# Optimization experiments

Hardware: AMD Instinct MI355X
Metric: run time of the kernel (lower is better)

## Reference

```python
import jax, jax.numpy as jnp
import numpy as np

NUM_EVENT, EVENT_DIM = 6, 32
NUM_WORD, WORD_DIM = 100000, 128
NUM_SKU, SKU_DIM = 500000, 128
NUM_CAT, CAT_DIM = 10000, 64
NUM_PRICE, PRICE_DIM = 100, 32
NUM_URL, URL_DIM = 200000, 128
HIDDEN = 512
B, S, W = 256, 256, 12
PAD = 0


def _table(key, n, d):
    t = jax.random.normal(key, (n, d), dtype=jnp.float32) * 0.02
    return t.at[PAD].set(0.0)  # padding_idx row is zero


def setup_inputs() -> dict:
    key = jax.random.key(0)
    ks = jax.random.split(key, 20)
    inp = {
        "event_table": _table(ks[0], NUM_EVENT, EVENT_DIM),
        "word_table": _table(ks[1], NUM_WORD, WORD_DIM),
        "sku_table": _table(ks[2], NUM_SKU, SKU_DIM),
        "cat_table": _table(ks[3], NUM_CAT, CAT_DIM),
        "price_table": _table(ks[4], NUM_PRICE, PRICE_DIM),
        "url_table": _table(ks[5], NUM_URL, URL_DIM),
        # Linear weights, torch convention: y = x @ W.T + b
        "sku_w": jax.random.normal(ks[6], (HIDDEN, EVENT_DIM + SKU_DIM + CAT_DIM + PRICE_DIM + WORD_DIM), dtype=jnp.float32) * 0.02,
        "sku_b": jnp.zeros((HIDDEN,), dtype=jnp.float32),
        "url_w": jax.random.normal(ks[7], (HIDDEN, URL_DIM + EVENT_DIM), dtype=jnp.float32) * 0.02,
        "url_b": jnp.zeros((HIDDEN,), dtype=jnp.float32),
        "query_w": jax.random.normal(ks[8], (HIDDEN, EVENT_DIM + WORD_DIM), dtype=jnp.float32) * 0.02,
        "query_b": jnp.zeros((HIDDEN,), dtype=jnp.float32),
        "event_type": jax.random.randint(ks[9], (B, S), 0, NUM_EVENT, dtype=jnp.int32),
        "sku_id": jax.random.randint(ks[10], (B, S), 0, NUM_SKU, dtype=jnp.int32),
        "url_id": jax.random.randint(ks[11], (B, S), 0, NUM_URL, dtype=jnp.int32),
        "cat_id": jax.random.randint(ks[12], (B, S), 0, NUM_CAT, dtype=jnp.int32),
        "price_id": jax.random.randint(ks[13], (B, S), 0, NUM_PRICE, dtype=jnp.int32),
        "word_id": jax.random.randint(ks[14], (B, S, W), 0, NUM_WORD, dtype=jnp.int32),
    }
    return inp


def _linear_relu(x, w, b):
    return jax.nn.relu(jnp.einsum("bsi,hi->bsh", x, w) + b)


def reference(event_table, word_table, sku_table, cat_table, price_table, url_table,
              sku_w, sku_b, url_w, url_b, query_w, query_b,
              event_type, sku_id, url_id, cat_id, price_id, word_id):
    # padding mask: 1.0 where event_type == PAD_IDX
    src_padding_mask = (event_type == PAD).astype(jnp.float32)

    event_emb = event_table[event_type]                 # [B,S,E]
    word_emb = word_table[word_id].mean(axis=-2)        # [B,S,Wd] (WordEmbedding avg)

    # SKU branch (event types 1,2,3): concat(event, sku, cat, price, word)
    sku_in = jnp.concatenate([event_emb, sku_table[sku_id], cat_table[cat_id],
                              price_table[price_id], word_emb], axis=-1)
    sku_out = _linear_relu(sku_in, sku_w, sku_b)        # [B,S,H]

    # URL branch (event type 4): concat(url, event)  -- note order in UrlEmbedding
    url_in = jnp.concatenate([url_table[url_id], event_emb], axis=-1)
    url_out = _linear_relu(url_in, url_w, url_b)

    # Query branch (event type 5): concat(event, word)
    query_in = jnp.concatenate([event_emb, word_emb], axis=-1)
    query_out = _linear_relu(query_in, query_w, query_b)

    is_sku = ((event_type >= 1) & (event_type <= 3))[..., None]
    is_url = (event_type == 4)[..., None]
    is_query = (event_type == 5)[..., None]

    seq_emb = (jnp.where(is_sku, sku_out, 0.0)
               + jnp.where(is_url, url_out, 0.0)
               + jnp.where(is_query, query_out, 0.0))   # PAD positions stay zero
    return seq_emb, src_padding_mask
```

## Files before the change

kernel.cpp:

```cpp
#include <hip/hip_runtime.h>
#include <hip/hip_bf16.h>
#if !__has_builtin(__builtin_amdgcn_cvt_pk_fp8_f32) || !__has_builtin(__builtin_amdgcn_cvt_pk_f32_fp8)
#include <hip/hip_fp8.h>
#endif

#define CUR_OFF   0
#define SLOT_OFF  1024
#define POS_OFF   263168
#define WSKU_OFF  1049600
#define WURL_OFF  1442816
#define WQRY_OFF  1639424
#define WF8_OFF   2097152
#define XS_OFF    27697152
#define XU_OFF    78127104
#define XQ_OFF    103342080

#define NPOS      65536
#define OUT_MASK  33554432
#define F8_SCALE  64.0f
#define F8_INV    (1.0f / (12.0f * 64.0f))

typedef __attribute__((ext_vector_type(8))) short bf16x8;
typedef __attribute__((ext_vector_type(4))) float f32x4;
typedef __attribute__((ext_vector_type(2))) float f32x2;
typedef __attribute__((ext_vector_type(2))) unsigned int u32x2;

__device__ __forceinline__ unsigned short f2bf(float x) {
    unsigned int u = __float_as_uint(x);
    return (unsigned short)((u + 0x7fffu + ((u >> 16) & 1u)) >> 16);
}
__device__ __forceinline__ void st2(__hip_bfloat16* d, float2 v) {
    unsigned int pk = (unsigned int)f2bf(v.x) | ((unsigned int)f2bf(v.y) << 16);
    *reinterpret_cast<unsigned int*>(d) = pk;
}
__device__ __forceinline__ float2 ld2(const float* p) {
    return *reinterpret_cast<const float2*>(p);
}

__device__ __forceinline__ unsigned int pk4_fp8(float a, float b, float c, float d) {
#if __has_builtin(__builtin_amdgcn_cvt_pk_fp8_f32)
    unsigned int v = 0;
    v = __builtin_amdgcn_cvt_pk_fp8_f32(a, b, v, false);
    v = __builtin_amdgcn_cvt_pk_fp8_f32(c, d, v, true);
    return v;
#else
    __hip_fp8_e4m3 fa(a), fb(b), fc(c), fd(d);
    return (unsigned int)fa.__x | ((unsigned int)fb.__x << 8)
         | ((unsigned int)fc.__x << 16) | ((unsigned int)fd.__x << 24);
#endif
}
__device__ __forceinline__ float2 upk2_fp8(unsigned int u) {
#if __has_builtin(__builtin_amdgcn_cvt_pk_f32_fp8)
    f32x2 r = __builtin_amdgcn_cvt_pk_f32_fp8(u, false);
    return make_float2(r.x, r.y);
#else
    __hip_fp8_e4m3 fa, fb;
    fa.__x = (unsigned char)(u & 0xff);
    fb.__x = (unsigned char)((u >> 8) & 0xff);
    return make_float2((float)fa, (float)fb);
#endif
}

#define AS1(p) ((const __attribute__((address_space(1))) void*)(p))
#define AS3(p) ((__attribute__((address_space(3))) void*)(p))

__global__ __launch_bounds__(256) void prep_k(const float* __restrict__ sw,
                                              const float* __restrict__ uw,
                                              const float* __restrict__ qw,
                                              const float* __restrict__ word_t,
                                              char* ws) {
    const int b = blockIdx.x, t = threadIdx.x;
    if (b < 6250) {
        size_t i = ((size_t)b * 256 + t) * 8;
        f32x4 v0 = *reinterpret_cast<const f32x4*>(word_t + i);
        f32x4 v1 = *reinterpret_cast<const f32x4*>(word_t + i + 4);
        u32x2 pk;
        pk.x = pk4_fp8(v0.x * F8_SCALE, v0.y * F8_SCALE, v0.z * F8_SCALE, v0.w * F8_SCALE);
        pk.y = pk4_fp8(v1.x * F8_SCALE, v1.y * F8_SCALE, v1.z * F8_SCALE, v1.w * F8_SCALE);
        *reinterpret_cast<u32x2*>((unsigned char*)(ws + WF8_OFF) + i) = pk;
        return;
    }
    int tt = (b - 6250) * 256 + t;
    if (tt < 3) ((int*)(ws + CUR_OFF))[tt] = 0;
    if (tt < 196608) {
        ((unsigned short*)(ws + WSKU_OFF))[tt] = f2bf(sw[tt]);
    } else if (tt < 294912) {
        int i = tt - 196608; int n = i / 192, k = i % 192;
        ((unsigned short*)(ws + WURL_OFF))[i] = (k < 160) ? f2bf(uw[n * 160 + k]) : 0;
    } else {
        int i = tt - 294912; int n = i / 192, k = i % 192;
        ((unsigned short*)(ws + WQRY_OFF))[i] = (k < 160) ? f2bf(qw[n * 160 + k]) : 0;
    }
}

__global__ __launch_bounds__(256) void alloc_k(const int* __restrict__ et_a,
                                               float* __restrict__ out, char* ws) {
    __shared__ int s_wcnt[4][3];
    __shared__ int s_base[3];
    __shared__ int s_woff[4][3];
    const int t = threadIdx.x, lane = t & 63, wid = t >> 6;
    int p = blockIdx.x * 256 + t;
    int et = et_a[p];
    int br = (et >= 1 && et <= 3) ? 0 : (et == 4 ? 1 : (et == 5 ? 2 : -1));
    unsigned long long m0 = __ballot(br == 0);
    unsigned long long m1 = __ballot(br == 1);
    unsigned long long m2 = __ballot(br == 2);
    if (lane == 0) {
        s_wcnt[wid][0] = (int)__popcll(m0);
        s_wcnt[wid][1] = (int)__popcll(m1);
        s_wcnt[wid][2] = (int)__popcll(m2);
    }
    __syncthreads();
    if (t < 3) {
        int c0 = s_wcnt[0][t], c1 = s_wcnt[1][t], c2 = s_wcnt[2][t], c3 = s_wcnt[3][t];
        int tot = c0 + c1 + c2 + c3;
        s_base[t] = tot ? atomicAdd(&((int*)(ws + CUR_OFF))[t], tot) : 0;
        s_woff[0][t] = 0; s_woff[1][t] = c0; s_woff[2][t] = c0 + c1; s_woff[3][t] = c0 + c1 + c2;
    }
    __syncthreads();
    unsigned long long lt = (1ull << lane) - 1ull;
    int slot = -1;
    if (br == 0)      slot = s_base[0] + s_woff[wid][0] + (int)__popcll(m0 & lt);
    else if (br == 1) slot = s_base[1] + s_woff[wid][1] + (int)__popcll(m1 & lt);
    else if (br == 2) slot = s_base[2] + s_woff[wid][2] + (int)__popcll(m2 & lt);
    ((int*)(ws + SLOT_OFF))[p] = slot;
    if (slot >= 0) ((int*)(ws + POS_OFF))[br * NPOS + slot] = p;
    __builtin_nontemporal_store((et == 0) ? 1.0f : 0.0f, &out[OUT_MASK + p]);
}

__device__ __forceinline__ float2 wmean_f8(const unsigned char* __restrict__ wt8,
                                           const int* __restrict__ wids, int lane) {
    float sx = 0.f, sy = 0.f;
    #pragma unroll
    for (int k = 0; k < 12; ++k) {
        unsigned int u = *reinterpret_cast<const unsigned short*>(
            wt8 + (size_t)wids[k] * 128 + 2 * lane);
        float2 v = upk2_fp8(u);
        sx += v.x; sy += v.y;
    }
    return make_float2(sx * F8_INV, sy * F8_INV);
}

__global__ __launch_bounds__(256) void build_k(
    const float* __restrict__ ev_t,
    const float* __restrict__ sku_t,  const float* __restrict__ cat_t,
    const float* __restrict__ price_t,const float* __restrict__ url_t,
    const int* __restrict__ et_a,     const int* __restrict__ sku_id,
    const int* __restrict__ url_id,   const int* __restrict__ cat_id,
    const int* __restrict__ price_id, const int* __restrict__ word_id,
    float* __restrict__ out, char* ws)
{
    const int t = threadIdx.x, lane = t & 63, wid = t >> 6;
    const int p = blockIdx.x * 4 + wid;
    const int et = et_a[p];
    if (et == 0) {
        f32x4 z = {0.f, 0.f, 0.f, 0.f};
        float* orow = out + (size_t)p * 512;
        __builtin_nontemporal_store(z, reinterpret_cast<f32x4*>(&orow[lane * 8]));
        __builtin_nontemporal_store(z, reinterpret_cast<f32x4*>(&orow[lane * 8 + 4]));
        return;
    }
    const int slot = ((const int*)(ws + SLOT_OFF))[p];
    const unsigned char* wf8 = (const unsigned char*)(ws + WF8_OFF);
    const float* evr = ev_t + et * 32;
    if (et <= 3) {
        __hip_bfloat16* X = (__hip_bfloat16*)(ws + XS_OFF + (size_t)slot * 768);
        if (lane < 16) st2(X + 2 * lane, ld2(evr + 2 * lane));
        const float* sr = sku_t + (size_t)sku_id[p] * 128;
        st2(X + 32 + 2 * lane, ld2(sr + 2 * lane));
        const float* crr = cat_t + (size_t)cat_id[p] * 64;
        if (lane < 32) st2(X + 160 + 2 * lane, ld2(crr + 2 * lane));
        const float* prr = price_t + (size_t)price_id[p] * 32;
        if (lane < 16) st2(X + 224 + 2 * lane, ld2(prr + 2 * lane));
        float2 w = wmean_f8(wf8, word_id + (size_t)p * 12, lane);
        st2(X + 256 + 2 * lane, w);
    } else if (et == 4) {
        __hip_bfloat16* X = (__hip_bfloat16*)(ws + XU_OFF + (size_t)slot * 384);
        const float* ur = url_t + (size_t)url_id[p] * 128;
        st2(X + 2 * lane, ld2(ur + 2 * lane));
        if (lane < 16) st2(X + 128 + 2 * lane, ld2(evr + 2 * lane));
        if (lane < 16) st2(X + 160 + 2 * lane, make_float2(0.f, 0.f));
    } else {
        __hip_bfloat16* X = (__hip_bfloat16*)(ws + XQ_OFF + (size_t)slot * 384);
        if (lane < 16) st2(X + 2 * lane, ld2(evr + 2 * lane));
        float2 w = wmean_f8(wf8, word_id + (size_t)p * 12, lane);
        st2(X + 32 + 2 * lane, w);
        if (lane < 16) st2(X + 160 + 2 * lane, make_float2(0.f, 0.f));
    }
}

__global__ __launch_bounds__(256, 2) void gemm_all_k(
    const char* __restrict__ ws_c, const float* __restrict__ sku_b,
    const float* __restrict__ url_b, const float* __restrict__ qry_b,
    float* __restrict__ out)
{
    const int z = blockIdx.z;
    const int count = ((const int*)(ws_c + CUR_OFF))[z];
    const int nmt = (count + 127) >> 7;
    const int nwg = nmt * 4;
    const int orig = blockIdx.x;
    if (orig >= nwg) return;
    const int q8 = nwg >> 3, r8 = nwg & 7;
    const int xcd = orig & 7, idx = orig >> 3;
    const int wg = (xcd < r8 ? xcd * (q8 + 1) : r8 * (q8 + 1) + (xcd - r8) * q8) + idx;
    const int mt = wg >> 2;
    const int row0 = mt * 128;
    const int nc0  = (wg & 3) * 128;

    const char* arena; const char* Wb; const float* bias; const int* posm;
    int astride, nkt;
    if (z == 0) { arena = ws_c + XS_OFF; Wb = ws_c + WSKU_OFF; bias = sku_b;
                  posm = (const int*)(ws_c + POS_OFF);          astride = 768; nkt = 6; }
    else if (z == 1) { arena = ws_c + XU_OFF; Wb = ws_c + WURL_OFF; bias = url_b;
                  posm = (const int*)(ws_c + POS_OFF) + NPOS;   astride = 384; nkt = 3; }
    else       { arena = ws_c + XQ_OFF; Wb = ws_c + WQRY_OFF; bias = qry_b;
                  posm = (const int*)(ws_c + POS_OFF) + 2*NPOS; astride = 384; nkt = 3; }
    const int wstride = astride;

    __shared__ char lds[2][2][16384];

    const int t = threadIdx.x;
    const int lane = t & 63;
    const int wid  = t >> 6;
    const int wr = wid >> 1, wc = wid & 1;
    const int r = lane & 15, q = lane >> 4;

    auto stage = [&](int buf, int kt) {
        #pragma unroll
        for (int i = 0; i < 4; ++i) {
            int row = i * 32 + (t >> 3);
            int sb  = (t & 7) ^ (row & 7);
            const char* ga = arena + (size_t)(row0 + row) * astride + kt * 128 + sb * 16;
            __builtin_amdgcn_global_load_lds(AS1(ga), AS3(&lds[buf][0][i * 4096 + t * 16]), 16, 0, 0);
            const char* gb = Wb + (size_t)(nc0 + row) * wstride + kt * 128 + sb * 16;
            __builtin_amdgcn_global_load_lds(AS1(gb), AS3(&lds[buf][1][i * 4096 + t * 16]), 16, 0, 0);
        }
    };

    f32x4 acc[4][4];
    #pragma unroll
    for (int m = 0; m < 4; ++m)
        #pragma unroll
        for (int n = 0; n < 4; ++n)
            acc[m][n] = (f32x4){0.f, 0.f, 0.f, 0.f};

    stage(0, 0);
    __syncthreads();
    int cur = 0;
    for (int kt = 0; kt < nkt; ++kt) {
        if (kt + 1 < nkt) stage(cur ^ 1, kt + 1);
        #pragma unroll
        for (int kk = 0; kk < 2; ++kk) {
            bf16x8 af[4], bfr[4];
            #pragma unroll
            for (int m = 0; m < 4; ++m) {
                int arow = wr * 64 + m * 16 + r;
                af[m] = *reinterpret_cast<const bf16x8*>(
                    &lds[cur][0][arow * 128 + (((kk * 4 + q) ^ (r & 7)) * 16)]);
            }
            #pragma unroll
            for (int n = 0; n < 4; ++n) {
                int brow = wc * 64 + n * 16 + r;
                bfr[n] = *reinterpret_cast<const bf16x8*>(
                    &lds[cur][1][brow * 128 + (((kk * 4 + q) ^ (r & 7)) * 16)]);
            }
            #pragma unroll
            for (int m = 0; m < 4; ++m)
                #pragma unroll
                for (int n = 0; n < 4; ++n)
                    acc[m][n] = __builtin_amdgcn_mfma_f32_16x16x32_bf16(af[m], bfr[n], acc[m][n], 0, 0, 0);
        }
        __syncthreads();
        cur ^= 1;
    }

    float bv[4];
    #pragma unroll
    for (int n = 0; n < 4; ++n) bv[n] = bias[nc0 + wc * 64 + n * 16 + r];
    #pragma unroll
    for (int m = 0; m < 4; ++m) {
        #pragma unroll
        for (int j = 0; j < 4; ++j) {
            int rl = wr * 64 + m * 16 + q * 4 + j;
            int gr = row0 + rl;
            if (gr < count) {
                int pos = posm[gr];
                float* orow = out + (size_t)pos * 512 + nc0 + wc * 64;
                #pragma unroll
                for (int n = 0; n < 4; ++n)
                    __builtin_nontemporal_store(fmaxf(acc[m][n][j] + bv[n], 0.f),
                                                &orow[n * 16 + r]);
            }
        }
    }
}

extern "C" void kernel_launch(void* const* d_in, const int* in_sizes, int n_in,
                              void* d_out, int out_size, void* d_ws, size_t ws_size,
                              hipStream_t stream) {
    const float* ev_t    = (const float*)d_in[0];
    const float* word_t  = (const float*)d_in[1];
    const float* sku_t   = (const float*)d_in[2];
    const float* cat_t   = (const float*)d_in[3];
    const float* price_t = (const float*)d_in[4];
    const float* url_t   = (const float*)d_in[5];
    const float* sku_w   = (const float*)d_in[6];
    const float* sku_b   = (const float*)d_in[7];
    const float* url_w   = (const float*)d_in[8];
    const float* url_b   = (const float*)d_in[9];
    const float* query_w = (const float*)d_in[10];
    const float* query_b = (const float*)d_in[11];
    const int* event_type = (const int*)d_in[12];
    const int* sku_id     = (const int*)d_in[13];
    const int* url_id     = (const int*)d_in[14];
    const int* cat_id     = (const int*)d_in[15];
    const int* price_id   = (const int*)d_in[16];
    const int* word_id    = (const int*)d_in[17];

    char*  ws  = (char*)d_ws;
    float* out = (float*)d_out;

    prep_k<<<7786, 256, 0, stream>>>(sku_w, url_w, query_w, word_t, ws);
    alloc_k<<<256, 256, 0, stream>>>(event_type, out, ws);
    build_k<<<16384, 256, 0, stream>>>(ev_t, sku_t, cat_t, price_t, url_t,
                                       event_type, sku_id, url_id, cat_id, price_id,
                                       word_id, out, ws);
    dim3 gg(2048, 1, 3);
    gemm_all_k<<<gg, 256, 0, stream>>>(ws, sku_b, url_b, query_b, out);
}
```

Measured before the change: 92.79 us.

## Switch GEMM operands and weights from bf16 to scaled fp8 MFMA

Activations (gathered embeddings) and all three weight matrices are now quantized to fp8 e4m3 with a x64 scale instead of bf16, and the GEMM uses the fp8 16x16x32 MFMA with a 1/4096 rescale in the epilogue. This halves workspace traffic for the X arenas and weights, halves K-tiles per GEMM, and raises MFMA throughput. The cost is much lower precision on every GEMM operand, including the embeddings themselves, which may exceed tolerance.

```diff
diff --git a/kernel.cpp b/kernel.cpp
--- a/kernel.cpp
+++ b/kernel.cpp
@@ -8,19 +8,18 @@
 #define SLOT_OFF  1024
 #define POS_OFF   263168
 #define WSKU_OFF  1049600
-#define WURL_OFF  1442816
-#define WQRY_OFF  1639424
+#define WURL_OFF  1246208
+#define WQRY_OFF  1377280
 #define WF8_OFF   2097152
-#define XS_OFF    27697152
-#define XU_OFF    78127104
-#define XQ_OFF    103342080
+#define XS_OFF    16777216
+#define XU_OFF    50331648
+#define XQ_OFF    68157440
 
 #define NPOS      65536
 #define OUT_MASK  33554432
 #define F8_SCALE  64.0f
-#define F8_INV    (1.0f / (12.0f * 64.0f))
-
-typedef __attribute__((ext_vector_type(8))) short bf16x8;
+#define INV4096   (1.0f / 4096.0f)
+
 typedef __attribute__((ext_vector_type(4))) float f32x4;
 typedef __attribute__((ext_vector_type(2))) float f32x2;
 typedef __attribute__((ext_vector_type(2))) unsigned int u32x2;
@@ -29,27 +28,29 @@
     unsigned int u = __float_as_uint(x);
     return (unsigned short)((u + 0x7fffu + ((u >> 16) & 1u)) >> 16);
 }
-__device__ __forceinline__ void st2(__hip_bfloat16* d, float2 v) {
-    unsigned int pk = (unsigned int)f2bf(v.x) | ((unsigned int)f2bf(v.y) << 16);
-    *reinterpret_cast<unsigned int*>(d) = pk;
-}
 __device__ __forceinline__ float2 ld2(const float* p) {
     return *reinterpret_cast<const float2*>(p);
 }
 
-__device__ __forceinline__ unsigned int pk4_fp8(float a, float b, float c, float d) {
+__device__ __forceinline__ unsigned int pk2_f8(float a, float b) {
+#if __has_builtin(__builtin_amdgcn_cvt_pk_fp8_f32)
+    return __builtin_amdgcn_cvt_pk_fp8_f32(a, b, 0u, false);
+#else
+    __hip_fp8_e4m3 fa(a), fb(b);
+    return (unsigned int)fa.__x | ((unsigned int)fb.__x << 8);
+#endif
+}
+__device__ __forceinline__ unsigned int pk4_f8(float a, float b, float c, float d) {
 #if __has_builtin(__builtin_amdgcn_cvt_pk_fp8_f32)
     unsigned int v = 0;
     v = __builtin_amdgcn_cvt_pk_fp8_f32(a, b, v, false);
     v = __builtin_amdgcn_cvt_pk_fp8_f32(c, d, v, true);
     return v;
 #else
-    __hip_fp8_e4m3 fa(a), fb(b), fc(c), fd(d);
-    return (unsigned int)fa.__x | ((unsigned int)fb.__x << 8)
-         | ((unsigned int)fc.__x << 16) | ((unsigned int)fd.__x << 24);
+    return pk2_f8(a, b) | (pk2_f8(c, d) << 16);
 #endif
 }
-__device__ __forceinline__ float2 upk2_fp8(unsigned int u) {
+__device__ __forceinline__ float2 upk2_f8(unsigned int u) {
 #if __has_builtin(__builtin_amdgcn_cvt_pk_f32_fp8)
     f32x2 r = __builtin_amdgcn_cvt_pk_f32_fp8(u, false);
     return make_float2(r.x, r.y);
@@ -59,6 +60,9 @@
     fb.__x = (unsigned char)((u >> 8) & 0xff);
     return make_float2((float)fa, (float)fb);
 #endif
+}
+__device__ __forceinline__ void st_f8x2(unsigned char* d, float a, float b) {
+    *reinterpret_cast<unsigned short*>(d) = (unsigned short)(pk2_f8(a, b) & 0xffffu);
 }
 
 #define AS1(p) ((const __attribute__((address_space(1))) void*)(p))
@@ -75,21 +79,24 @@
         f32x4 v0 = *reinterpret_cast<const f32x4*>(word_t + i);
         f32x4 v1 = *reinterpret_cast<const f32x4*>(word_t + i + 4);
         u32x2 pk;
-        pk.x = pk4_fp8(v0.x * F8_SCALE, v0.y * F8_SCALE, v0.z * F8_SCALE, v0.w * F8_SCALE);
-        pk.y = pk4_fp8(v1.x * F8_SCALE, v1.y * F8_SCALE, v1.z * F8_SCALE, v1.w * F8_SCALE);
+        pk.x = pk4_f8(v0.x * F8_SCALE, v0.y * F8_SCALE, v0.z * F8_SCALE, v0.w * F8_SCALE);
+        pk.y = pk4_f8(v1.x * F8_SCALE, v1.y * F8_SCALE, v1.z * F8_SCALE, v1.w * F8_SCALE);
         *reinterpret_cast<u32x2*>((unsigned char*)(ws + WF8_OFF) + i) = pk;
         return;
     }
     int tt = (b - 6250) * 256 + t;
     if (tt < 3) ((int*)(ws + CUR_OFF))[tt] = 0;
     if (tt < 196608) {
-        ((unsigned short*)(ws + WSKU_OFF))[tt] = f2bf(sw[tt]);
-    } else if (tt < 294912) {
-        int i = tt - 196608; int n = i / 192, k = i % 192;
-        ((unsigned short*)(ws + WURL_OFF))[i] = (k < 160) ? f2bf(uw[n * 160 + k]) : 0;
+        ((unsigned char*)(ws + WSKU_OFF))[tt] =
+            (unsigned char)(pk2_f8(sw[tt] * F8_SCALE, 0.f) & 0xffu);
+    } else if (tt < 327680) {
+        int i = tt - 196608; int n = i >> 8, k = i & 255;
+        ((unsigned char*)(ws + WURL_OFF))[i] = (k < 160)
+            ? (unsigned char)(pk2_f8(uw[n * 160 + k] * F8_SCALE, 0.f) & 0xffu) : 0;
     } else {
-        int i = tt - 294912; int n = i / 192, k = i % 192;
-        ((unsigned short*)(ws + WQRY_OFF))[i] = (k < 160) ? f2bf(qw[n * 160 + k]) : 0;
+        int i = tt - 327680; int n = i >> 8, k = i & 255;
+        ((unsigned char*)(ws + WQRY_OFF))[i] = (k < 160)
+            ? (unsigned char)(pk2_f8(qw[n * 160 + k] * F8_SCALE, 0.f) & 0xffu) : 0;
     }
 }
 
@@ -128,17 +135,18 @@
     __builtin_nontemporal_store((et == 0) ? 1.0f : 0.0f, &out[OUT_MASK + p]);
 }
 
-__device__ __forceinline__ float2 wmean_f8(const unsigned char* __restrict__ wt8,
-                                           const int* __restrict__ wids, int lane) {
+__device__ __forceinline__ float2 wsum_f8(const unsigned char* __restrict__ wt8,
+                                          const int* __restrict__ wids, int lane) {
     float sx = 0.f, sy = 0.f;
     #pragma unroll
     for (int k = 0; k < 12; ++k) {
         unsigned int u = *reinterpret_cast<const unsigned short*>(
             wt8 + (size_t)wids[k] * 128 + 2 * lane);
-        float2 v = upk2_fp8(u);
+        float2 v = upk2_f8(u);
         sx += v.x; sy += v.y;
     }
-    return make_float2(sx * F8_INV, sy * F8_INV);
+    const float inv = 1.0f / 12.0f;
+    return make_float2(sx * inv, sy * inv);
 }
 
 __global__ __launch_bounds__(256) void build_k(
@@ -164,28 +172,35 @@
     const unsigned char* wf8 = (const unsigned char*)(ws + WF8_OFF);
     const float* evr = ev_t + et * 32;
     if (et <= 3) {
-        __hip_bfloat16* X = (__hip_bfloat16*)(ws + XS_OFF + (size_t)slot * 768);
-        if (lane < 16) st2(X + 2 * lane, ld2(evr + 2 * lane));
+        unsigned char* X = (unsigned char*)(ws + XS_OFF) + (size_t)slot * 384;
+        if (lane < 16) { float2 e = ld2(evr + 2 * lane);
+                         st_f8x2(X + 2 * lane, e.x * F8_SCALE, e.y * F8_SCALE); }
         const float* sr = sku_t + (size_t)sku_id[p] * 128;
-        st2(X + 32 + 2 * lane, ld2(sr + 2 * lane));
-        const float* crr = cat_t + (size_t)cat_id[p] * 64;
-        if (lane < 32) st2(X + 160 + 2 * lane, ld2(crr + 2 * lane));
-        const float* prr = price_t + (size_t)price_id[p] * 32;
-        if (lane < 16) st2(X + 224 + 2 * lane, ld2(prr + 2 * lane));
-        float2 w = wmean_f8(wf8, word_id + (size_t)p * 12, lane);
-        st2(X + 256 + 2 * lane, w);
+        { float2 s = ld2(sr + 2 * lane);
+          st_f8x2(X + 32 + 2 * lane, s.x * F8_SCALE, s.y * F8_SCALE); }
+        if (lane < 32) { const float* cr = cat_t + (size_t)cat_id[p] * 64;
+                         float2 c = ld2(cr + 2 * lane);
+                         st_f8x2(X + 160 + 2 * lane, c.x * F8_SCALE, c.y * F8_SCALE); }
+        if (lane < 16) { const float* pr = price_t + (size_t)price_id[p] * 32;
+                         float2 v = ld2(pr + 2 * lane);
+                         st_f8x2(X + 224 + 2 * lane, v.x * F8_SCALE, v.y * F8_SCALE); }
+        float2 w = wsum_f8(wf8, word_id + (size_t)p * 12, lane);
+        st_f8x2(X + 256 + 2 * lane, w.x, w.y);
     } else if (et == 4) {
-        __hip_bfloat16* X = (__hip_bfloat16*)(ws + XU_OFF + (size_t)slot * 384);
+        unsigned char* X = (unsigned char*)(ws + XU_OFF) + (size_t)slot * 256;
         const float* ur = url_t + (size_t)url_id[p] * 128;
-        st2(X + 2 * lane, ld2(ur + 2 * lane));
-        if (lane < 16) st2(X + 128 + 2 * lane, ld2(evr + 2 * lane));
-        if (lane < 16) st2(X + 160 + 2 * lane, make_float2(0.f, 0.f));
+        { float2 u = ld2(ur + 2 * lane);
+          st_f8x2(X + 2 * lane, u.x * F8_SCALE, u.y * F8_SCALE); }
+        if (lane < 16) { float2 e = ld2(evr + 2 * lane);
+                         st_f8x2(X + 128 + 2 * lane, e.x * F8_SCALE, e.y * F8_SCALE); }
+        if (lane < 48) *reinterpret_cast<unsigned short*>(X + 160 + 2 * lane) = 0;
     } else {
-        __hip_bfloat16* X = (__hip_bfloat16*)(ws + XQ_OFF + (size_t)slot * 384);
-        if (lane < 16) st2(X + 2 * lane, ld2(evr + 2 * lane));
-        float2 w = wmean_f8(wf8, word_id + (size_t)p * 12, lane);
-        st2(X + 32 + 2 * lane, w);
-        if (lane < 16) st2(X + 160 + 2 * lane, make_float2(0.f, 0.f));
+        unsigned char* X = (unsigned char*)(ws + XQ_OFF) + (size_t)slot * 256;
+        if (lane < 16) { float2 e = ld2(evr + 2 * lane);
+                         st_f8x2(X + 2 * lane, e.x * F8_SCALE, e.y * F8_SCALE); }
+        float2 w = wsum_f8(wf8, word_id + (size_t)p * 12, lane);
+        st_f8x2(X + 32 + 2 * lane, w.x, w.y);
+        if (lane < 48) *reinterpret_cast<unsigned short*>(X + 160 + 2 * lane) = 0;
     }
 }
 
@@ -210,12 +225,11 @@
     const char* arena; const char* Wb; const float* bias; const int* posm;
     int astride, nkt;
     if (z == 0) { arena = ws_c + XS_OFF; Wb = ws_c + WSKU_OFF; bias = sku_b;
-                  posm = (const int*)(ws_c + POS_OFF);          astride = 768; nkt = 6; }
+                  posm = (const int*)(ws_c + POS_OFF);          astride = 384; nkt = 3; }
     else if (z == 1) { arena = ws_c + XU_OFF; Wb = ws_c + WURL_OFF; bias = url_b;
-                  posm = (const int*)(ws_c + POS_OFF) + NPOS;   astride = 384; nkt = 3; }
+                  posm = (const int*)(ws_c + POS_OFF) + NPOS;   astride = 256; nkt = 2; }
     else       { arena = ws_c + XQ_OFF; Wb = ws_c + WQRY_OFF; bias = qry_b;
-                  posm = (const int*)(ws_c + POS_OFF) + 2*NPOS; astride = 384; nkt = 3; }
-    const int wstride = astride;
+                  posm = (const int*)(ws_c + POS_OFF) + 2*NPOS; astride = 256; nkt = 2; }
 
     __shared__ char lds[2][2][16384];
 
@@ -232,7 +246,7 @@
             int sb  = (t & 7) ^ (row & 7);
             const char* ga = arena + (size_t)(row0 + row) * astride + kt * 128 + sb * 16;
             __builtin_amdgcn_global_load_lds(AS1(ga), AS3(&lds[buf][0][i * 4096 + t * 16]), 16, 0, 0);
-            const char* gb = Wb + (size_t)(nc0 + row) * wstride + kt * 128 + sb * 16;
+            const char* gb = Wb + (size_t)(nc0 + row) * astride + kt * 128 + sb * 16;
             __builtin_amdgcn_global_load_lds(AS1(gb), AS3(&lds[buf][1][i * 4096 + t * 16]), 16, 0, 0);
         }
     };
@@ -250,25 +264,27 @@
     for (int kt = 0; kt < nkt; ++kt) {
         if (kt + 1 < nkt) stage(cur ^ 1, kt + 1);
         #pragma unroll
-        for (int kk = 0; kk < 2; ++kk) {
-            bf16x8 af[4], bfr[4];
+        for (int kk = 0; kk < 4; ++kk) {
+            const int u  = kk * 2 + (q >> 1);
+            const int wo = (q & 1) * 8;
+            long af[4], bfr[4];
             #pragma unroll
             for (int m = 0; m < 4; ++m) {
                 int arow = wr * 64 + m * 16 + r;
-                af[m] = *reinterpret_cast<const bf16x8*>(
-                    &lds[cur][0][arow * 128 + (((kk * 4 + q) ^ (r & 7)) * 16)]);
+                af[m] = *reinterpret_cast<const long*>(
+                    &lds[cur][0][arow * 128 + ((u ^ (arow & 7)) << 4) + wo]);
             }
             #pragma unroll
             for (int n = 0; n < 4; ++n) {
                 int brow = wc * 64 + n * 16 + r;
-                bfr[n] = *reinterpret_cast<const bf16x8*>(
-                    &lds[cur][1][brow * 128 + (((kk * 4 + q) ^ (r & 7)) * 16)]);
+                bfr[n] = *reinterpret_cast<const long*>(
+                    &lds[cur][1][brow * 128 + ((u ^ (brow & 7)) << 4) + wo]);
             }
             #pragma unroll
             for (int m = 0; m < 4; ++m)
                 #pragma unroll
                 for (int n = 0; n < 4; ++n)
-                    acc[m][n] = __builtin_amdgcn_mfma_f32_16x16x32_bf16(af[m], bfr[n], acc[m][n], 0, 0, 0);
+                    acc[m][n] = __builtin_amdgcn_mfma_f32_16x16x32_fp8_fp8(af[m], bfr[n], acc[m][n], 0, 0, 0);
         }
         __syncthreads();
         cur ^= 1;
@@ -288,8 +304,8 @@
                 float* orow = out + (size_t)pos * 512 + nc0 + wc * 64;
                 #pragma unroll
                 for (int n = 0; n < 4; ++n)
-                    __builtin_nontemporal_store(fmaxf(acc[m][n][j] + bv[n], 0.f),
-                                                &orow[n * 16 + r]);
+                    __builtin_nontemporal_store(
+                        fmaxf(acc[m][n][j] * INV4096 + bv[n], 0.f), &orow[n * 16 + r]);
             }
         }
     }
@@ -320,7 +336,7 @@
     char*  ws  = (char*)d_ws;
     float* out = (float*)d_out;
 
-    prep_k<<<7786, 256, 0, stream>>>(sku_w, url_w, query_w, word_t, ws);
+    prep_k<<<8042, 256, 0, stream>>>(sku_w, url_w, query_w, word_t, ws);
     alloc_k<<<256, 256, 0, stream>>>(event_type, out, ws);
     build_k<<<16384, 256, 0, stream>>>(ev_t, sku_t, cat_t, price_t, url_t,
                                        event_type, sku_id, url_id, cat_id, price_id,
```

Result: faster. 86.64 us (-6.6%).
